# Performance work log

Measured on AMD Instinct MI355X. Metric: run time of the kernel, lower is better.

## Reference

```python
import jax, jax.numpy as jnp
import numpy as np


def _conv(x, w, b, stride=1):
    # NCHW conv, 3x3 kernel, padding=1
    y = jax.lax.conv_general_dilated(
        x, w, (stride, stride), [(1, 1), (1, 1)],
        dimension_numbers=("NCHW", "OIHW", "NCHW"))
    return y + b[None, :, None, None]


def setup_inputs() -> dict:
    key = jax.random.key(0)
    ks = jax.random.split(key, 13)
    s = 0.05
    d = jnp.float32
    return {
        "x": jax.random.normal(ks[0], (1, 3, 512, 512), d),
        "low0_w": jax.random.normal(ks[1], (64, 3, 3, 3), d) * s,
        "low0_b": jax.random.normal(ks[2], (64,), d) * s,
        "ll_rh_w": jax.random.normal(ks[3], (4, 61, 61, 3, 3), d) * s,
        "ll_rh_b": jax.random.normal(ks[4], (4, 61), d) * s,
        "ll_lh_w": jax.random.normal(ks[5], (4, 3, 3, 3, 3), d) * s,
        "ll_lh_b": jax.random.normal(ks[6], (4, 3), d) * s,
        "hl0_w": jax.random.normal(ks[7], (64, 61, 3, 3), d) * s,
        "hl0_b": jax.random.normal(ks[8], (64,), d) * s,
        "hl_w": jax.random.normal(ks[9], (3, 64, 64, 3, 3), d) * s,
        "hl_b": jax.random.normal(ks[10], (3, 64), d) * s,
        "lin_w": jax.random.normal(ks[11], (30, 64), d) * s,
        "lin_b": jax.random.normal(ks[12], (30,), d) * s,
    }


def reference(x, low0_w, low0_b, ll_rh_w, ll_rh_b, ll_lh_w, ll_lh_b,
              hl0_w, hl0_b, hl_w, hl_b, lin_w, lin_b):
    # ---- low-level path: 64-channel full-resolution features ----
    I = _conv(x, low0_w, low0_b)  # (b,64,H,W)
    for i in range(ll_rh_w.shape[0]):
        rh = jax.nn.relu(_conv(I[:, :61], ll_rh_w[i], ll_rh_b[i]))
        lh = jnp.tanh(_conv(I[:, 61:], ll_lh_w[i], ll_lh_b[i]))
        I = jnp.concatenate([rh, lh], axis=1)
    # ---- high-level path: predicts 30 params -> 3x10 color transform ----
    h = _conv(I[:, :61], hl0_w, hl0_b)
    for i in range(hl_w.shape[0]):
        h = jax.nn.relu(_conv(h, hl_w[i], hl_b[i], stride=2))
        h = jax.lax.reduce_window(h, -jnp.inf, jax.lax.max,
                                  (1, 1, 2, 2), (1, 1, 2, 2), "VALID")
    g = h.mean(axis=(2, 3))            # (b,64) global average pool
    Wp = g @ lin_w.T + lin_b           # (b,30)
    Wm = Wp.reshape(3, 10)             # batch=1, matches torch reshape
    # ---- vectorized Tform: per-pixel quadratic feature expansion ----
    I3 = I[:, 61:]                     # (b,3,H,W)
    r, gc, bc = I3[:, 0], I3[:, 1], I3[:, 2]
    feats = jnp.stack([r * r, r * gc, r * bc, r,
                       gc * gc, gc * bc, gc,
                       bc * bc, bc, jnp.ones_like(r)], axis=1)  # (b,10,H,W)
    return jnp.einsum("ok,bkhw->bohw", Wm, feats)  # (b,3,H,W)
```

## Files before the change

kernel.cpp:

```cpp
#include <hip/hip_runtime.h>
#include <cstdint>

typedef _Float16 half8 __attribute__((ext_vector_type(8)));
typedef float f32x4 __attribute__((ext_vector_type(4)));

#define HW_ (512*512)

__global__ __launch_bounds__(256)
void pre_k(const float* __restrict__ x, const float* __restrict__ low0_w,
           const float* __restrict__ low0_b,
           const float* __restrict__ rh_w, const float* __restrict__ hl0_w,
           const float* __restrict__ hl_w, _Float16* __restrict__ M,
           float* __restrict__ L, _Float16* __restrict__ wt,
           _Float16* __restrict__ zg)
{
    __shared__ float tile[3 * 324];
    if (blockIdx.x < 144) {
        if (blockIdx.x == 0 && threadIdx.x < 32) zg[threadIdx.x] = (_Float16)0.f;
        int t = blockIdx.x * 256 + threadIdx.x;
        if (t >= 8 * 4608) return;
        int layer = t / 4608;
        int r = t - layer * 4608;
        int lane = r & 63, ci = r >> 6;
        int m = ci & 3, kk = (ci >> 2) & 1, s = ci >> 3;
        int o = m * 16 + (lane & 15);
        int cb = kk * 32 + ((lane >> 4) & 3) * 8;
        const float* w; int O, CIN;
        if (layer < 4)      { w = rh_w + (size_t)layer * 61 * 61 * 9; O = 61; CIN = 61; }
        else if (layer == 4){ w = hl0_w;                              O = 64; CIN = 61; }
        else                { w = hl_w + (size_t)(layer - 5) * 64 * 64 * 9; O = 64; CIN = 64; }
        half8 v;
        #pragma unroll
        for (int j = 0; j < 8; ++j) {
            int c = cb + j;
            float f = (o < O && c < CIN) ? w[((size_t)o * CIN + c) * 9 + s] : 0.f;
            v[j] = (_Float16)f;
        }
        *(half8*)(wt + (size_t)layer * 36864 + (size_t)r * 8) = v;
        return;
    }

    const int id = blockIdx.x - 144;
    const int bx = id & 31, by = (id >> 5) & 31, z = id >> 10;
    const int tx = threadIdx.x & 15, ty = threadIdx.x >> 4;
    const int ox = bx * 16 + tx, oy = by * 16 + ty;
    const int ix0 = bx * 16 - 1, iy0 = by * 16 - 1;

    for (int i = threadIdx.x; i < 3 * 324; i += 256) {
        int c = i / 324, p = i - c * 324;
        int iy = p / 18, ix = p - iy * 18;
        int gy = iy0 + iy, gx = ix0 + ix;
        float v = 0.f;
        if ((unsigned)gy < 512u && (unsigned)gx < 512u)
            v = x[(size_t)c * HW_ + (size_t)gy * 512 + gx];
        tile[i] = v;
    }
    __syncthreads();

    float p9[3][9];
    #pragma unroll
    for (int c = 0; c < 3; ++c)
        #pragma unroll
        for (int dy = 0; dy < 3; ++dy)
            #pragma unroll
            for (int dx = 0; dx < 3; ++dx)
                p9[c][dy * 3 + dx] = tile[c * 324 + (ty + dy) * 18 + tx + dx];

    float acc[16];
    #pragma unroll
    for (int o = 0; o < 16; ++o) {
        int oc = z * 16 + o;
        float a = low0_b[oc];
        const float* wo = low0_w + (size_t)oc * 27;
        #pragma unroll
        for (int c = 0; c < 3; ++c)
            #pragma unroll
            for (int k = 0; k < 9; ++k)
                a = fmaf(p9[c][k], wo[c * 9 + k], a);
        acc[o] = a;
    }

    const size_t pix = (size_t)oy * 512 + ox;
    half8 h0, h1;
    #pragma unroll
    for (int o = 0; o < 8; ++o) { h0[o] = (_Float16)acc[o]; h1[o] = (_Float16)acc[8 + o]; }
    _Float16* orow = M + pix * 64 + z * 16;
    *(half8*)(orow)     = h0;
    *(half8*)(orow + 8) = h1;
    if (z == 3) {
        #pragma unroll
        for (int o = 13; o < 16; ++o)
            L[(size_t)(o - 13) * HW_ + pix] = acc[o];
    }
}

template<int O, int ACT, int DOLH>
__global__ __launch_bounds__(256, 2)
void conv_mfma_k(const _Float16* __restrict__ in, const _Float16* __restrict__ wt,
                 const float* __restrict__ bias, _Float16* __restrict__ out,
                 const float* __restrict__ L_in, const float* __restrict__ lhw,
                 const float* __restrict__ lhb, float* __restrict__ L_out,
                 const _Float16* __restrict__ zg)
{
    __shared__ _Float16 __attribute__((aligned(16))) in_t[2592 * 8];
    __shared__ _Float16 __attribute__((aligned(16))) wbuf[3][4096];
    const int tid = threadIdx.x;
    const int l = tid & 63, wv = tid >> 6;
    const int px = l & 15, g = l >> 4;
    const int orig = blockIdx.x;
    const int id = ((orig & 7) << 7) + (orig >> 3);
    const int bx = id & 31, by = id >> 5;
    const int iy0 = by * 16 - 1, ix0 = bx * 16 - 1;

    #pragma unroll
    for (int k = 0; k < 11; ++k) {
        int i = tid + (k << 8);
        if (i < 2592) {
            int p = i >> 3, jl = i & 7;
            int iy = p / 18, ix = p - iy * 18;
            int gy = iy0 + iy, gx = ix0 + ix;
            int j = jl ^ (p & 7);
            const _Float16* src = ((unsigned)gy < 512u && (unsigned)gx < 512u)
                ? in + ((size_t)gy * 512 + gx) * 64 + j * 8 : zg;
            __builtin_amdgcn_global_load_lds(
                (const __attribute__((address_space(1))) void*)src,
                (__attribute__((address_space(3))) void*)(in_t + (size_t)(i - l) * 8),
                16, 0, 0);
        }
    }
    #pragma unroll
    for (int tp = 0; tp < 2; ++tp) {
        #pragma unroll
        for (int it = 0; it < 2; ++it) {
            int ci = (it << 8) + tid;
            __builtin_amdgcn_global_load_lds(
                (const __attribute__((address_space(1))) void*)(wt + (size_t)tp * 4096 + ci * 8),
                (__attribute__((address_space(3))) void*)(wbuf[tp] + (size_t)(ci - l) * 8),
                16, 0, 0);
        }
    }
    __syncthreads();

    float bs[4][4];
    #pragma unroll
    for (int m = 0; m < 4; ++m)
        #pragma unroll
        for (int r = 0; r < 4; ++r) {
            int o = m * 16 + g * 4 + r;
            bs[m][r] = (o < O) ? bias[o] : 0.f;
        }

    f32x4 acc[4][4];
    #pragma unroll
    for (int m = 0; m < 4; ++m)
        #pragma unroll
        for (int f = 0; f < 4; ++f) acc[m][f] = (f32x4){0.f, 0.f, 0.f, 0.f};

    #pragma unroll
    for (int s = 0; s < 9; ++s) {
        if (s < 7) {
            #pragma unroll
            for (int it = 0; it < 2; ++it) {
                int ci = (it << 8) + tid;
                __builtin_amdgcn_global_load_lds(
                    (const __attribute__((address_space(1))) void*)(wt + (size_t)(s + 2) * 4096 + ci * 8),
                    (__attribute__((address_space(3))) void*)(wbuf[(s + 2) % 3] + (size_t)(ci - l) * 8),
                    16, 0, 0);
            }
        }
        const _Float16* wb = wbuf[s % 3];
        half8 a[8];
        #pragma unroll
        for (int q = 0; q < 8; ++q)
            a[q] = *(const half8*)(wb + (q << 9) + l * 8);

        const int dy = s / 3, dx = s - dy * 3;
        #pragma unroll
        for (int f = 0; f < 4; ++f) {
            int ipix = (4 * wv + f + dy) * 18 + px + dx;
            int rb = ipix * 64, sw = (ipix & 7) << 3;
            #pragma unroll
            for (int kk = 0; kk < 2; ++kk) {
                half8 b = *(const half8*)&in_t[rb + ((kk * 32 + g * 8) ^ sw)];
                #pragma unroll
                for (int m = 0; m < 4; ++m)
                    acc[m][f] = __builtin_amdgcn_mfma_f32_16x16x32_f16(
                        a[kk * 4 + m], b, acc[m][f], 0, 0, 0);
            }
        }
        __builtin_amdgcn_sched_barrier(0);
        if (s < 7) asm volatile("s_waitcnt vmcnt(2)" ::: "memory");
        else       asm volatile("s_waitcnt vmcnt(0)" ::: "memory");
        __builtin_amdgcn_s_barrier();
        asm volatile("" ::: "memory");
    }

    #pragma unroll
    for (int f = 0; f < 4; ++f) {
        const int p = (4 * wv + f) * 16 + px;
        const int sw = p & 7;
        #pragma unroll
        for (int m = 0; m < 4; ++m) {
            union { _Float16 h[4]; uint2 u; } pk;
            #pragma unroll
            for (int r = 0; r < 4; ++r) {
                int o = m * 16 + g * 4 + r;
                float v = acc[m][f][r] + bs[m][r];
                if (ACT) v = fmaxf(v, 0.f);
                pk.h[r] = (o < O) ? (_Float16)v : (_Float16)0.f;
            }
            int chunk = (m * 2 + (g >> 1)) ^ sw;
            *(uint2*)&in_t[p * 64 + chunk * 8 + (g & 1) * 4] = pk.u;
        }
    }
    __syncthreads();
    #pragma unroll
    for (int k = 0; k < 8; ++k) {
        int q = (k << 8) + tid;
        int p = q >> 3, jc = q & 7;
        half8 v = *(const half8*)&in_t[p * 64 + ((jc ^ (p & 7)) * 8)];
        int row = p >> 4, col = p & 15;
        _Float16* dst = out + (((size_t)(by * 16 + row) * 512) + bx * 16 + col) * 64 + jc * 8;
        *(half8*)dst = v;
    }

    if (DOLH) {
        const int tx = tid & 15, ty = tid >> 4;
        const int oy = by * 16 + ty, ox = bx * 16 + tx;
        float pv[27];
        #pragma unroll
        for (int c = 0; c < 3; ++c)
            #pragma unroll
            for (int d2 = 0; d2 < 9; ++d2) {
                int gy = oy + d2 / 3 - 1, gx = ox + d2 % 3 - 1;
                pv[c * 9 + d2] = ((unsigned)gy < 512u && (unsigned)gx < 512u)
                    ? L_in[(size_t)c * HW_ + (size_t)gy * 512 + gx] : 0.f;
            }
        const size_t pix = (size_t)oy * 512 + ox;
        #pragma unroll
        for (int oc = 0; oc < 3; ++oc) {
            float a = lhb[oc];
            #pragma unroll
            for (int k = 0; k < 27; ++k)
                a = fmaf(pv[k], lhw[oc * 27 + k], a);
            L_out[(size_t)oc * HW_ + pix] = tanhf(a);
        }
    }
}

template<int FP32OUT, int NB>
__global__ __launch_bounds__(256, 3)
void conv_s2_pool_k(const _Float16* __restrict__ in, int Hin,
                    const _Float16* __restrict__ wt,
                    const float* __restrict__ bias, void* __restrict__ outv,
                    const _Float16* __restrict__ zg)
{
    const int Hp = Hin >> 2;
    __shared__ _Float16 __attribute__((aligned(16))) in_t[2312 * 8];
    __shared__ _Float16 __attribute__((aligned(16))) wbuf[2][4096];
    const int tid = threadIdx.x;
    const int l = tid & 63, wv = tid >> 6;
    const int n = l & 15, g = l >> 4;
    int id = blockIdx.x;
    if (NB == 32) id = ((id & 7) << 7) + (id >> 3);
    const int bx = id % NB, by = id / NB;
    const int iy0 = by * 16 - 1, ix0 = bx * 16 - 1;

    #pragma unroll
    for (int k = 0; k < 10; ++k) {
        int i = tid + (k << 8);
        if (i < 2312) {
            int p = i >> 3, jl = i & 7;
            int iy = p / 17, ix = p - iy * 17;
            int gy = iy0 + iy, gx = ix0 + ix;
            int j = jl ^ (p & 7);
            const _Float16* src =
                ((unsigned)gy < (unsigned)Hin && (unsigned)gx < (unsigned)Hin)
                    ? in + ((size_t)gy * Hin + gx) * 64 + j * 8 : zg;
            __builtin_amdgcn_global_load_lds(
                (const __attribute__((address_space(1))) void*)src,
                (__attribute__((address_space(3))) void*)(in_t + (size_t)(i - l) * 8),
                16, 0, 0);
        }
    }
    #pragma unroll
    for (int it = 0; it < 2; ++it) {
        int ci = (it << 8) + tid;
        __builtin_amdgcn_global_load_lds(
            (const __attribute__((address_space(1))) void*)(wt + ci * 8),
            (__attribute__((address_space(3))) void*)(wbuf[0] + (size_t)(ci - l) * 8),
            16, 0, 0);
    }
    __syncthreads();

    float bs[4];
    #pragma unroll
    for (int r = 0; r < 4; ++r) bs[r] = bias[wv * 16 + g * 4 + r];

    f32x4 acc[4];
    #pragma unroll
    for (int f = 0; f < 4; ++f) acc[f] = (f32x4){0.f, 0.f, 0.f, 0.f};

    const int py_lo = n >> 3, pxc = n & 7;
    #pragma unroll
    for (int s = 0; s < 9; ++s) {
        if (s < 8) {
            #pragma unroll
            for (int it = 0; it < 2; ++it) {
                int ci = (it << 8) + tid;
                __builtin_amdgcn_global_load_lds(
                    (const __attribute__((address_space(1))) void*)(wt + ((s + 1) << 12) + ci * 8),
                    (__attribute__((address_space(3))) void*)(wbuf[(s + 1) & 1] + (size_t)(ci - l) * 8),
                    16, 0, 0);
            }
        }
        const _Float16* wb = wbuf[s & 1];
        half8 a[2];
        #pragma unroll
        for (int kk = 0; kk < 2; ++kk)
            a[kk] = *(const half8*)(wb + ((kk * 4 + wv) << 9) + l * 8);

        const int dy = s / 3, dx = s - dy * 3;
        #pragma unroll
        for (int f = 0; f < 4; ++f) {
            int py = 2 * f + py_lo;
            int ipix = (2 * py + dy) * 17 + 2 * pxc + dx;
            int rb = ipix * 64, sw = (ipix & 7) << 3;
            #pragma unroll
            for (int kk = 0; kk < 2; ++kk) {
                half8 b = *(const half8*)&in_t[rb + ((kk * 32 + g * 8) ^ sw)];
                acc[f] = __builtin_amdgcn_mfma_f32_16x16x32_f16(a[kk], b, acc[f], 0, 0, 0);
            }
        }
        __syncthreads();
    }

    #pragma unroll
    for (int f = 0; f < 4; ++f)
        #pragma unroll
        for (int r = 0; r < 4; ++r) {
            float v = fmaxf(acc[f][r] + bs[r], 0.f);
            v = fmaxf(v, __shfl_xor(v, 1));
            v = fmaxf(v, __shfl_xor(v, 8));
            if ((l & 9) == 0) {
                int o = wv * 16 + g * 4 + r;
                size_t pp = ((size_t)(by * 4 + f) * Hp + bx * 4 + (n >> 1)) * 64 + o;
                if (FP32OUT) ((float*)outv)[pp] = v;
                else         ((_Float16*)outv)[pp] = (_Float16)v;
            }
        }
}

__global__ __launch_bounds__(256)
void final_k(const float* __restrict__ P2, const float* __restrict__ lw,
             const float* __restrict__ lb, const float* __restrict__ I3,
             float* __restrict__ out)
{
    __shared__ float part[256];
    __shared__ float g[64];
    __shared__ float W[30];
    const int t = threadIdx.x;
    {
        int c = t >> 2, q = t & 3;
        float s = 0.f;
        #pragma unroll
        for (int k = 0; k < 16; ++k)
            s += P2[(q * 16 + k) * 64 + c];
        part[t] = s;
    }
    __syncthreads();
    if (t < 64)
        g[t] = (part[t * 4] + part[t * 4 + 1] + part[t * 4 + 2] + part[t * 4 + 3])
               * (1.f / 64.f);
    __syncthreads();
    if (t < 30) {
        float s = lb[t];
        #pragma unroll
        for (int c = 0; c < 64; ++c) s = fmaf(g[c], lw[t * 64 + c], s);
        W[t] = s;
    }
    __syncthreads();

    const int HW = 512 * 512;
    for (int i = blockIdx.x * blockDim.x + t; i < HW;
         i += gridDim.x * blockDim.x) {
        float r = I3[i], gc = I3[HW + i], b = I3[2 * HW + i];
        float f[10] = { r * r, r * gc, r * b, r, gc * gc, gc * b, gc, b * b, b, 1.f };
        #pragma unroll
        for (int o = 0; o < 3; ++o) {
            float s = 0.f;
            #pragma unroll
            for (int k = 0; k < 10; ++k) s = fmaf(W[o * 10 + k], f[k], s);
            out[(size_t)o * HW + i] = s;
        }
    }
}

extern "C" void kernel_launch(void* const* d_in, const int* in_sizes, int n_in,
                              void* d_out, int out_size, void* d_ws, size_t ws_size,
                              hipStream_t stream)
{
    const float* x      = (const float*)d_in[0];
    const float* low0_w = (const float*)d_in[1];
    const float* low0_b = (const float*)d_in[2];
    const float* rh_w   = (const float*)d_in[3];
    const float* rh_b   = (const float*)d_in[4];
    const float* lh_w   = (const float*)d_in[5];
    const float* lh_b   = (const float*)d_in[6];
    const float* hl0_w  = (const float*)d_in[7];
    const float* hl0_b  = (const float*)d_in[8];
    const float* hl_w   = (const float*)d_in[9];
    const float* hl_b   = (const float*)d_in[10];
    const float* lin_w  = (const float*)d_in[11];
    const float* lin_b  = (const float*)d_in[12];
    float* out = (float*)d_out;

    const size_t HW = 512 * 512;
    _Float16* M0 = (_Float16*)d_ws;
    _Float16* M1 = M0 + (size_t)64 * HW;
    _Float16* P0 = M1 + (size_t)64 * HW;
    _Float16* P1 = P0 + (size_t)16384 * 64;
    _Float16* WT = P1 + (size_t)1024 * 64;
    _Float16* ZG = WT + (size_t)8 * 36864;
    float*    P2 = (float*)(ZG + 32);
    float*    L0 = P2 + 64 * 64;
    float*    L1 = L0 + (size_t)3 * HW;

    dim3 blk(256);

    pre_k<<<dim3(4240), blk, 0, stream>>>(x, low0_w, low0_b,
                                          rh_w, hl0_w, hl_w, M0, L0, WT, ZG);

    _Float16* cur = M0; _Float16* nxt = M1;
    float* Lc = L0; float* Ln = L1;
    for (int i = 0; i < 4; ++i) {
        conv_mfma_k<61, 1, 1><<<dim3(1024), blk, 0, stream>>>(
            cur, WT + (size_t)i * 36864, rh_b + i * 61, nxt,
            Lc, lh_w + (size_t)i * 81, lh_b + i * 3, Ln, ZG);
        _Float16* t = cur; cur = nxt; nxt = t;
        float* tl = Lc; Lc = Ln; Ln = tl;
    }

    conv_mfma_k<64, 0, 0><<<dim3(1024), blk, 0, stream>>>(
        cur, WT + (size_t)4 * 36864, hl0_b, nxt,
        nullptr, nullptr, nullptr, nullptr, ZG);

    conv_s2_pool_k<0, 32><<<dim3(1024), blk, 0, stream>>>(
        nxt, 512, WT + (size_t)5 * 36864, hl_b, (void*)P0, ZG);
    conv_s2_pool_k<0, 8><<<dim3(64), blk, 0, stream>>>(
        P0, 128, WT + (size_t)6 * 36864, hl_b + 64, (void*)P1, ZG);
    conv_s2_pool_k<1, 2><<<dim3(4), blk, 0, stream>>>(
        P1, 32, WT + (size_t)7 * 36864, hl_b + 128, (void*)P2, ZG);

    final_k<<<dim3(2048), blk, 0, stream>>>(P2, lin_w, lin_b, Lc, out);
}
```

Measured before the change: 210.0 us.

## Halve weight staging buffers and split K loop to fit three blocks per CU

The MFMA conv kernel's weight ring buffer is cut to half size by streaming weights in 18 half-tap phases (one K-half per phase) instead of 9 full taps. Launch bounds are raised from 2 to 3 blocks per CU, so LDS and register use must shrink. The goal is higher occupancy to hide memory and barrier latency. In exchange it doubles the number of block-wide barriers and waitcnt stalls, and it may force register spills under the tighter budget.

```diff
diff --git a/kernel.cpp b/kernel.cpp
--- a/kernel.cpp
+++ b/kernel.cpp
@@ -95,7 +95,7 @@
 }
 
 template<int O, int ACT, int DOLH>
-__global__ __launch_bounds__(256, 2)
+__global__ __launch_bounds__(256, 3)
 void conv_mfma_k(const _Float16* __restrict__ in, const _Float16* __restrict__ wt,
                  const float* __restrict__ bias, _Float16* __restrict__ out,
                  const float* __restrict__ L_in, const float* __restrict__ lhw,
@@ -103,7 +103,7 @@
                  const _Float16* __restrict__ zg)
 {
     __shared__ _Float16 __attribute__((aligned(16))) in_t[2592 * 8];
-    __shared__ _Float16 __attribute__((aligned(16))) wbuf[3][4096];
+    __shared__ _Float16 __attribute__((aligned(16))) wbuf[3][2048];
     const int tid = threadIdx.x;
     const int l = tid & 63, wv = tid >> 6;
     const int px = l & 15, g = l >> 4;
@@ -130,14 +130,10 @@
     }
     #pragma unroll
     for (int tp = 0; tp < 2; ++tp) {
-        #pragma unroll
-        for (int it = 0; it < 2; ++it) {
-            int ci = (it << 8) + tid;
-            __builtin_amdgcn_global_load_lds(
-                (const __attribute__((address_space(1))) void*)(wt + (size_t)tp * 4096 + ci * 8),
-                (__attribute__((address_space(3))) void*)(wbuf[tp] + (size_t)(ci - l) * 8),
-                16, 0, 0);
-        }
+        __builtin_amdgcn_global_load_lds(
+            (const __attribute__((address_space(1))) void*)(wt + (size_t)tp * 2048 + tid * 8),
+            (__attribute__((address_space(3))) void*)(wbuf[tp] + (size_t)(tid - l) * 8),
+            16, 0, 0);
     }
     __syncthreads();
 
@@ -157,40 +153,34 @@
         for (int f = 0; f < 4; ++f) acc[m][f] = (f32x4){0.f, 0.f, 0.f, 0.f};
 
     #pragma unroll
-    for (int s = 0; s < 9; ++s) {
-        if (s < 7) {
-            #pragma unroll
-            for (int it = 0; it < 2; ++it) {
-                int ci = (it << 8) + tid;
-                __builtin_amdgcn_global_load_lds(
-                    (const __attribute__((address_space(1))) void*)(wt + (size_t)(s + 2) * 4096 + ci * 8),
-                    (__attribute__((address_space(3))) void*)(wbuf[(s + 2) % 3] + (size_t)(ci - l) * 8),
-                    16, 0, 0);
-            }
-        }
-        const _Float16* wb = wbuf[s % 3];
-        half8 a[8];
-        #pragma unroll
-        for (int q = 0; q < 8; ++q)
-            a[q] = *(const half8*)(wb + (q << 9) + l * 8);
-
+    for (int ph = 0; ph < 18; ++ph) {
+        if (ph < 16) {
+            __builtin_amdgcn_global_load_lds(
+                (const __attribute__((address_space(1))) void*)(wt + (size_t)(ph + 2) * 2048 + tid * 8),
+                (__attribute__((address_space(3))) void*)(wbuf[(ph + 2) % 3] + (size_t)(tid - l) * 8),
+                16, 0, 0);
+        }
+        const int s = ph >> 1, kk = ph & 1;
         const int dy = s / 3, dx = s - dy * 3;
+        const _Float16* wb = wbuf[ph % 3];
+        half8 a[4];
+        #pragma unroll
+        for (int m = 0; m < 4; ++m)
+            a[m] = *(const half8*)(wb + (m << 9) + l * 8);
+
         #pragma unroll
         for (int f = 0; f < 4; ++f) {
             int ipix = (4 * wv + f + dy) * 18 + px + dx;
             int rb = ipix * 64, sw = (ipix & 7) << 3;
-            #pragma unroll
-            for (int kk = 0; kk < 2; ++kk) {
-                half8 b = *(const half8*)&in_t[rb + ((kk * 32 + g * 8) ^ sw)];
-                #pragma unroll
-                for (int m = 0; m < 4; ++m)
-                    acc[m][f] = __builtin_amdgcn_mfma_f32_16x16x32_f16(
-                        a[kk * 4 + m], b, acc[m][f], 0, 0, 0);
-            }
+            half8 b = *(const half8*)&in_t[rb + ((kk * 32 + g * 8) ^ sw)];
+            #pragma unroll
+            for (int m = 0; m < 4; ++m)
+                acc[m][f] = __builtin_amdgcn_mfma_f32_16x16x32_f16(
+                    a[m], b, acc[m][f], 0, 0, 0);
         }
         __builtin_amdgcn_sched_barrier(0);
-        if (s < 7) asm volatile("s_waitcnt vmcnt(2)" ::: "memory");
-        else       asm volatile("s_waitcnt vmcnt(0)" ::: "memory");
+        if (ph < 16) asm volatile("s_waitcnt vmcnt(1)" ::: "memory");
+        else         asm volatile("s_waitcnt vmcnt(0)" ::: "memory");
         __builtin_amdgcn_s_barrier();
         asm volatile("" ::: "memory");
     }
```

Result: slower. 225.4 us (+7.3%).
